# Optimization experiments

Hardware: AMD Instinct MI355X
Metric: run time of the kernel (lower is better)

The kernel has to match this reference:

```python
import jax, jax.numpy as jnp
import numpy as np

N = 2048
RESTITUTION = 0.5
EPS = 1e-12


def setup_inputs() -> dict:
    key = jax.random.key(0)
    k1, k2, k3, k4 = jax.random.split(key, 4)
    pos = jax.random.uniform(k1, (N, 2), jnp.float32, 0.0, 200.0)
    rad = jax.random.uniform(k2, (N,), jnp.float32, 0.5, 2.0)
    vel = jax.random.normal(k3, (N, 2), jnp.float32)
    mass = jax.random.uniform(k4, (N,), jnp.float32, 0.5, 2.0)
    return {"pos": pos, "rad": rad, "vel": vel, "mass": mass, "seed": 0}


def _forward(pos, rad, vel, mass, seed):
    rkey = jax.random.key(seed)
    skey = jax.random.split(rkey)[0]  # mirrors skey = jr.split(rkey)[0]
    # ---- pairwise circle-vs-circle contact tests, lower triangle i > j ----
    d = pos[:, None, :] - pos[None, :, :]            # [N,N,2], vector j -> i
    dist = jnp.sqrt(jnp.sum(d * d, -1) + EPS)        # [N,N]
    pen = (rad[:, None] + rad[None, :]) - dist       # penetration depth
    tri = jnp.arange(N)[:, None] > jnp.arange(N)[None, :]
    valid = (pen > 0.0) & tri                        # i < j pairs are nan'd in original
    normal = d / dist[..., None]
    pen_vec_raw = normal * pen[..., None]            # [N,N,2]
    cp_raw = 0.5 * (pos[:, None, :] + pos[None, :, :])  # contact point (midpoint)
    # scatter counts of non-nan contacts (computed in original, unused downstream)
    counts = valid.astype(jnp.int32)
    # ---- bernoulli(0.5)-gated recording into all_contacts ----
    skey = jax.random.split(skey)[0]
    gkey, _ = jax.random.split(skey)
    gate = jax.random.bernoulli(gkey, 0.5, (N, N))
    keep = valid & gate
    all_pen = jnp.where(keep[..., None], pen_vec_raw, 0.0)   # init zeros
    all_cp = jnp.where(keep[..., None], cp_raw, jnp.nan)     # init nan
    # ---- per-row uniform random choice among recorded (non-nan) contacts ----
    ok = ~jnp.any(jnp.isnan(all_cp), axis=-1)        # [N,N]
    n_ok = jnp.sum(ok, axis=-1)                      # [N]
    logits = jnp.where(ok, 0.0, -jnp.inf)
    keys = jax.random.split(skey, N)
    sampled = jax.vmap(jax.random.categorical)(keys, logits)  # uniform over valid
    rows = jnp.arange(N)
    chosen_j = jnp.where(n_ok == 0, rows, sampled)   # fall back to self (skipped)
    pen_sel = all_pen[rows, chosen_j]                # [N,2]
    cp_sel = all_cp[rows, chosen_j]                  # [N,2]
    inv_m = 1.0 / mass

    # ---- sequential collision resolution (scatter updates into SoA) ----
    def step(carry, x):
        p, v = carry
        i, j, pv, cp = x
        upd = (i != j) & ~jnp.any(jnp.isnan(cp))
        pi, pj = p[i], p[j]
        vi, vj = v[i], v[j]
        imi, imj = inv_m[i], inv_m[j]
        nrm = pv / (jnp.sqrt(jnp.sum(pv * pv) + EPS))
        corr = pv / (imi + imj)                      # positional de-penetration
        new_pi = pi + corr * imi
        new_pj = pj - corr * imj
        vrel = jnp.dot(vi - vj, nrm)
        jimp = jnp.where(vrel < 0.0, -(1.0 + RESTITUTION) * vrel / (imi + imj), 0.0)
        new_vi = vi + jimp * imi * nrm
        new_vj = vj - jimp * imj * nrm
        p = p.at[i].set(jnp.where(upd, new_pi, pi))
        p = p.at[j].set(jnp.where(upd, new_pj, pj))
        v = v.at[i].set(jnp.where(upd, new_vi, vi))
        v = v.at[j].set(jnp.where(upd, new_vj, vj))
        return (p, v), None

    (pos_out, vel_out), _ = jax.lax.scan(step, (pos, vel), (rows, chosen_j, pen_sel, cp_sel))
    return jnp.concatenate([pos_out, vel_out], axis=-1)  # [N,4]


def reference(pos, rad, vel, mass, seed):
    return _forward(pos, rad, vel, mass, seed)
```

## Files before the change

kernel.cpp:

```cpp
#include <hip/hip_runtime.h>
#include <stdint.h>

#define NPART 2048
#define FEPS 1e-12f
#define PARTITIONABLE 1

__device__ __forceinline__ uint32_t rotl32(uint32_t v, uint32_t r) {
  return (v << r) | (v >> (32u - r));
}

__device__ __forceinline__ void tf2x32(uint32_t k0, uint32_t k1,
                                       uint32_t x0, uint32_t x1,
                                       uint32_t& o0, uint32_t& o1) {
  uint32_t ks2 = k0 ^ k1 ^ 0x1BD11BDAu;
#define TF_RND(r) { x0 += x1; x1 = rotl32(x1, r); x1 ^= x0; }
  x0 += k0; x1 += k1;
  TF_RND(13u) TF_RND(15u) TF_RND(26u) TF_RND(6u)
  x0 += k1; x1 += ks2 + 1u;
  TF_RND(17u) TF_RND(29u) TF_RND(16u) TF_RND(24u)
  x0 += ks2; x1 += k0 + 2u;
  TF_RND(13u) TF_RND(15u) TF_RND(26u) TF_RND(6u)
  x0 += k0; x1 += k1 + 3u;
  TF_RND(17u) TF_RND(29u) TF_RND(16u) TF_RND(24u)
  x0 += k1; x1 += ks2 + 4u;
  TF_RND(13u) TF_RND(15u) TF_RND(26u) TF_RND(6u)
  x0 += ks2; x1 += k0 + 5u;
#undef TF_RND
  o0 = x0; o1 = x1;
}

__device__ __forceinline__ void split_first(uint32_t k0, uint32_t k1,
                                            uint32_t& o0, uint32_t& o1) {
#if PARTITIONABLE
  tf2x32(k0, k1, 0u, 0u, o0, o1);
#else
  uint32_t a0, a1, b0, b1;
  tf2x32(k0, k1, 0u, 2u, a0, a1);
  tf2x32(k0, k1, 1u, 3u, b0, b1);
  o0 = a0; o1 = b0;
#endif
}

__device__ __forceinline__ void split_at(uint32_t k0, uint32_t k1, uint32_t M,
                                         uint32_t r, uint32_t& o0, uint32_t& o1) {
#if PARTITIONABLE
  tf2x32(k0, k1, 0u, r, o0, o1);
#else
  uint32_t c0 = 2u * r, c1 = 2u * r + 1u;
  uint32_t a0, a1;
  if (c0 < M) { tf2x32(k0, k1, c0, c0 + M, a0, a1); o0 = a0; }
  else        { tf2x32(k0, k1, c0 - M, c0, a0, a1); o0 = a1; }
  if (c1 < M) { tf2x32(k0, k1, c1, c1 + M, a0, a1); o1 = a0; }
  else        { tf2x32(k0, k1, c1 - M, c1, a0, a1); o1 = a1; }
#endif
}

__device__ __forceinline__ uint32_t bits_at(uint32_t k0, uint32_t k1,
                                            uint32_t S_half, uint32_t idx) {
  uint32_t a0, a1;
#if PARTITIONABLE
  (void)S_half;
  tf2x32(k0, k1, 0u, idx, a0, a1);
  return a0 ^ a1;
#else
  if (idx < S_half) { tf2x32(k0, k1, idx, idx + S_half, a0, a1); return a0; }
  else              { tf2x32(k0, k1, idx - S_half, idx, a0, a1); return a1; }
#endif
}

__device__ __forceinline__ void derive_keys(int seed, uint32_t& g0, uint32_t& g1,
                                            uint32_t& s0, uint32_t& s1) {
  uint64_t sv = (uint64_t)(int64_t)seed;
  uint32_t k0 = (uint32_t)(sv >> 32), k1 = (uint32_t)sv;
  uint32_t a0, a1;
  split_first(k0, k1, a0, a1);
  split_first(a0, a1, s0, s1);
  split_first(s0, s1, g0, g1);
}

__global__ __launch_bounds__(256) void phase1_choose(
    const float* __restrict__ pos, const float* __restrict__ rad,
    const int* __restrict__ seedp, int* __restrict__ chosen,
    float* __restrict__ pen_out) {
#pragma clang fp contract(off)
  const int lane = threadIdx.x & 63;
  const int i = blockIdx.x * 4 + (threadIdx.x >> 6);

  uint32_t g0, g1, s0, s1;
  derive_keys(seedp[0], g0, g1, s0, s1);
  uint32_t ki0, ki1;
  split_at(s0, s1, (uint32_t)NPART, (uint32_t)i, ki0, ki1);

  const float pix = pos[2 * i], piy = pos[2 * i + 1];
  const float ri = rad[i];

  unsigned long long best = 0ull;
  for (int j = lane; j < i; j += 64) {
    float2 pj = reinterpret_cast<const float2*>(pos)[j];
    float dx = pix - pj.x;
    float dy = piy - pj.y;
    float dist = sqrtf(dx * dx + dy * dy + FEPS);
    float pen = (ri + rad[j]) - dist;
    if (pen > 0.0f) {
      uint32_t gb = bits_at(g0, g1, (uint32_t)NPART * NPART / 2u,
                            (uint32_t)(i * NPART + j));
      if ((gb >> 31) == 0u) {
        uint32_t b = bits_at(ki0, ki1, (uint32_t)NPART / 2u, (uint32_t)j);
        unsigned long long cand =
            ((unsigned long long)(b >> 9) << 32) |
            (uint32_t)(0xFFFFFFFFu - (uint32_t)j);
        if (cand > best) best = cand;
      }
    }
  }
  for (int off = 1; off < 64; off <<= 1) {
    unsigned long long o = __shfl_xor(best, off, 64);
    if (o > best) best = o;
  }
  if (lane == 0) {
    if (best == 0ull) {
      chosen[i] = -1;
      pen_out[2 * i] = 0.0f;
      pen_out[2 * i + 1] = 0.0f;
    } else {
      int j = (int)(0xFFFFFFFFu - (uint32_t)(best & 0xFFFFFFFFu));
      float2 pj = reinterpret_cast<const float2*>(pos)[j];
      float dx = pix - pj.x;
      float dy = piy - pj.y;
      float dist = sqrtf(dx * dx + dy * dy + FEPS);
      float pen = (ri + rad[j]) - dist;
      chosen[i] = j;
      pen_out[2 * i] = (dx / dist) * pen;
      pen_out[2 * i + 1] = (dy / dist) * pen;
    }
  }
}

__global__ __launch_bounds__(256) void phase2_scan(
    const float* __restrict__ pos, const float* __restrict__ vel,
    const float* __restrict__ mass, const int* __restrict__ chosen,
    const float* __restrict__ pen, float* __restrict__ out) {
#pragma clang fp contract(off)
  __shared__ float px[NPART], py[NPART], vx[NPART], vy[NPART];
  __shared__ int list_[NPART], cjl[NPART];
  __shared__ float Ax[NPART], Ay[NPART], Bx[NPART], By[NPART];
  __shared__ float nx_[NPART], ny_[NPART], ss[NPART], imi_[NPART], imj_[NPART];
  __shared__ int minK[NPART];
  __shared__ unsigned char done[NPART];
  __shared__ int cnts[256];
  __shared__ int total, remaining;

  const int tid = threadIdx.x;
  for (int r = tid; r < NPART; r += 256) {
    float2 p2 = reinterpret_cast<const float2*>(pos)[r];
    float2 v2 = reinterpret_cast<const float2*>(vel)[r];
    px[r] = p2.x; py[r] = p2.y;
    vx[r] = v2.x; vy[r] = v2.y;
  }

  const int base = tid * 8;
  int loc[8];
  int c = 0;
#pragma unroll
  for (int t = 0; t < 8; ++t) {
    loc[t] = chosen[base + t];
    if (loc[t] >= 0) c++;
  }
  cnts[tid] = c;
  __syncthreads();
  for (int off = 1; off < 256; off <<= 1) {
    int v = 0;
    if (tid >= off) v = cnts[tid - off];
    __syncthreads();
    cnts[tid] += v;
    __syncthreads();
  }
  int excl = cnts[tid] - c;
  if (tid == 255) total = cnts[255];
  __syncthreads();
  {
    int w = excl;
#pragma unroll
    for (int t = 0; t < 8; ++t) {
      if (loc[t] >= 0) { list_[w] = base + t; cjl[w] = loc[t]; w++; }
    }
  }
  __syncthreads();
  const int K = total;

  for (int k = tid; k < K; k += 256) {
    int i = list_[k], j = cjl[k];
    float imi = 1.0f / mass[i];
    float imj = 1.0f / mass[j];
    float s = imi + imj;
    float pvx = pen[2 * i], pvy = pen[2 * i + 1];
    float nn = sqrtf(pvx * pvx + pvy * pvy + FEPS);
    Ax[k] = (pvx / s) * imi; Ay[k] = (pvy / s) * imi;
    Bx[k] = (pvx / s) * imj; By[k] = (pvy / s) * imj;
    nx_[k] = pvx / nn; ny_[k] = pvy / nn;
    ss[k] = s; imi_[k] = imi; imj_[k] = imj;
  }
  for (int k = tid; k < K; k += 256) done[k] = 0;
  if (tid == 0) remaining = K;
  __syncthreads();

  for (int round = 0; round < NPART; ++round) {
    for (int p = tid; p < NPART; p += 256) minK[p] = 0x7FFFFFFF;
    __syncthreads();
    for (int k = tid; k < K; k += 256) {
      if (!done[k]) {
        atomicMin(&minK[list_[k]], k);
        atomicMin(&minK[cjl[k]], k);
      }
    }
    __syncthreads();
    for (int k = tid; k < K; k += 256) {
      if (!done[k]) {
        int i = list_[k], j = cjl[k];
        if (minK[i] == k && minK[j] == k) {
          px[i] = px[i] + Ax[k]; py[i] = py[i] + Ay[k];
          px[j] = px[j] - Bx[k]; py[j] = py[j] - By[k];
          float rx = vx[i] - vx[j], ry = vy[i] - vy[j];
          float vrel = rx * nx_[k] + ry * ny_[k];
          if (vrel < 0.0f) {
            float jimp = (-1.5f * vrel) / ss[k];
            float ji = jimp * imi_[k], jj = jimp * imj_[k];
            vx[i] = vx[i] + ji * nx_[k]; vy[i] = vy[i] + ji * ny_[k];
            vx[j] = vx[j] - jj * nx_[k]; vy[j] = vy[j] - jj * ny_[k];
          }
          done[k] = 1;
          atomicSub(&remaining, 1);
        }
      }
    }
    __syncthreads();
    if (remaining == 0) break;
  }

  for (int r = tid; r < NPART; r += 256) {
    float4 o;
    o.x = px[r]; o.y = py[r]; o.z = vx[r]; o.w = vy[r];
    reinterpret_cast<float4*>(out)[r] = o;
  }
}

extern "C" void kernel_launch(void* const* d_in, const int* in_sizes, int n_in,
                              void* d_out, int out_size, void* d_ws, size_t ws_size,
                              hipStream_t stream) {
  const float* pos = (const float*)d_in[0];
  const float* rad = (const float*)d_in[1];
  const float* vel = (const float*)d_in[2];
  const float* mass = (const float*)d_in[3];
  const int* seed = (const int*)d_in[4];

  int* chosen = (int*)d_ws;
  float* pen = (float*)((char*)d_ws + NPART * sizeof(int));

  phase1_choose<<<dim3(NPART / 4), dim3(256), 0, stream>>>(pos, rad, seed,
                                                           chosen, pen);
  phase2_scan<<<dim3(1), dim3(256), 0, stream>>>(pos, vel, mass, chosen, pen,
                                                 (float*)d_out);
}
```

Before: 85.27 us.

## Run collision rounds in a single wavefront with round-tagged atomics

Phase 2 now runs the conflict-free round scheduling in one 64-lane wavefront, so the per-round block barriers and minK reset are replaced by round-tagged atomicMax and a wave vote. Shared arrays are packed into float2/float4 and a combined i|j index, and the block prefix scan is replaced with wave shuffles. Phase 1 remaps rows so each block handles rows spread across the triangle, to balance work per block. The active-set bitmask only covers up to 32 slots per lane, which caps K at 2048, and only one wave does the update work.

New measurement: 83.94 us. About the same (-1.6%).

```diff
diff --git a/kernel.cpp b/kernel.cpp
--- a/kernel.cpp
+++ b/kernel.cpp
@@ -84,7 +84,7 @@
     float* __restrict__ pen_out) {
 #pragma clang fp contract(off)
   const int lane = threadIdx.x & 63;
-  const int i = blockIdx.x * 4 + (threadIdx.x >> 6);
+  const int i = blockIdx.x + 512 * (threadIdx.x >> 6);
 
   uint32_t g0, g1, s0, s1;
   derive_keys(seedp[0], g0, g1, s0, s1);
@@ -141,106 +141,121 @@
     const float* __restrict__ mass, const int* __restrict__ chosen,
     const float* __restrict__ pen, float* __restrict__ out) {
 #pragma clang fp contract(off)
-  __shared__ float px[NPART], py[NPART], vx[NPART], vy[NPART];
-  __shared__ int list_[NPART], cjl[NPART];
-  __shared__ float Ax[NPART], Ay[NPART], Bx[NPART], By[NPART];
-  __shared__ float nx_[NPART], ny_[NPART], ss[NPART], imi_[NPART], imj_[NPART];
+  __shared__ float2 pxy[NPART], vxy[NPART];
+  __shared__ int ij[NPART];
+  __shared__ float4 PA[NPART];
+  __shared__ float4 PB[NPART];
   __shared__ int minK[NPART];
-  __shared__ unsigned char done[NPART];
-  __shared__ int cnts[256];
-  __shared__ int total, remaining;
+  __shared__ int wsum[4];
 
   const int tid = threadIdx.x;
+  const int lane = tid & 63, w = tid >> 6;
+
   for (int r = tid; r < NPART; r += 256) {
-    float2 p2 = reinterpret_cast<const float2*>(pos)[r];
-    float2 v2 = reinterpret_cast<const float2*>(vel)[r];
-    px[r] = p2.x; py[r] = p2.y;
-    vx[r] = v2.x; vy[r] = v2.y;
+    pxy[r] = reinterpret_cast<const float2*>(pos)[r];
+    vxy[r] = reinterpret_cast<const float2*>(vel)[r];
+    minK[r] = 0;
   }
 
   const int base = tid * 8;
-  int loc[8];
+  int4 c0 = reinterpret_cast<const int4*>(chosen)[2 * tid];
+  int4 c1 = reinterpret_cast<const int4*>(chosen)[2 * tid + 1];
+  int loc[8] = {c0.x, c0.y, c0.z, c0.w, c1.x, c1.y, c1.z, c1.w};
   int c = 0;
 #pragma unroll
-  for (int t = 0; t < 8; ++t) {
-    loc[t] = chosen[base + t];
-    if (loc[t] >= 0) c++;
-  }
-  cnts[tid] = c;
-  __syncthreads();
-  for (int off = 1; off < 256; off <<= 1) {
-    int v = 0;
-    if (tid >= off) v = cnts[tid - off];
-    __syncthreads();
-    cnts[tid] += v;
-    __syncthreads();
-  }
-  int excl = cnts[tid] - c;
-  if (tid == 255) total = cnts[255];
-  __syncthreads();
+  for (int t = 0; t < 8; ++t) c += (loc[t] >= 0);
+
+  int incl = c;
+#pragma unroll
+  for (int off = 1; off < 64; off <<= 1) {
+    int v = __shfl_up(incl, off, 64);
+    if (lane >= off) incl += v;
+  }
+  if (lane == 63) wsum[w] = incl;
+  __syncthreads();
+  int woff = 0, K = 0;
+#pragma unroll
+  for (int q = 0; q < 4; ++q) {
+    int s = wsum[q];
+    if (q < w) woff += s;
+    K += s;
+  }
   {
-    int w = excl;
+    int wr = woff + incl - c;
 #pragma unroll
     for (int t = 0; t < 8; ++t) {
-      if (loc[t] >= 0) { list_[w] = base + t; cjl[w] = loc[t]; w++; }
-    }
-  }
-  __syncthreads();
-  const int K = total;
+      if (loc[t] >= 0) { ij[wr] = ((base + t) << 16) | loc[t]; wr++; }
+    }
+  }
+  __syncthreads();
 
   for (int k = tid; k < K; k += 256) {
-    int i = list_[k], j = cjl[k];
+    int pr = ij[k];
+    int i = pr >> 16, j = pr & 0xFFFF;
     float imi = 1.0f / mass[i];
     float imj = 1.0f / mass[j];
     float s = imi + imj;
     float pvx = pen[2 * i], pvy = pen[2 * i + 1];
     float nn = sqrtf(pvx * pvx + pvy * pvy + FEPS);
-    Ax[k] = (pvx / s) * imi; Ay[k] = (pvy / s) * imi;
-    Bx[k] = (pvx / s) * imj; By[k] = (pvy / s) * imj;
-    nx_[k] = pvx / nn; ny_[k] = pvy / nn;
-    ss[k] = s; imi_[k] = imi; imj_[k] = imj;
-  }
-  for (int k = tid; k < K; k += 256) done[k] = 0;
-  if (tid == 0) remaining = K;
-  __syncthreads();
-
-  for (int round = 0; round < NPART; ++round) {
-    for (int p = tid; p < NPART; p += 256) minK[p] = 0x7FFFFFFF;
-    __syncthreads();
-    for (int k = tid; k < K; k += 256) {
-      if (!done[k]) {
-        atomicMin(&minK[list_[k]], k);
-        atomicMin(&minK[cjl[k]], k);
-      }
-    }
-    __syncthreads();
-    for (int k = tid; k < K; k += 256) {
-      if (!done[k]) {
-        int i = list_[k], j = cjl[k];
-        if (minK[i] == k && minK[j] == k) {
-          px[i] = px[i] + Ax[k]; py[i] = py[i] + Ay[k];
-          px[j] = px[j] - Bx[k]; py[j] = py[j] - By[k];
-          float rx = vx[i] - vx[j], ry = vy[i] - vy[j];
-          float vrel = rx * nx_[k] + ry * ny_[k];
-          if (vrel < 0.0f) {
-            float jimp = (-1.5f * vrel) / ss[k];
-            float ji = jimp * imi_[k], jj = jimp * imj_[k];
-            vx[i] = vx[i] + ji * nx_[k]; vy[i] = vy[i] + ji * ny_[k];
-            vx[j] = vx[j] - jj * nx_[k]; vy[j] = vy[j] - jj * ny_[k];
-          }
-          done[k] = 1;
-          atomicSub(&remaining, 1);
+    PA[k] = make_float4((pvx / s) * imi, (pvy / s) * imi,
+                        (pvx / s) * imj, (pvy / s) * imj);
+    PB[k] = make_float4(pvx / nn, pvy / nn, imi, imj);
+  }
+  __syncthreads();
+
+  if (w == 0) {
+    const int RMAX = (K + 63) >> 6;
+    uint32_t act = 0;
+    for (int r = 0; r < RMAX; ++r)
+      if (r * 64 + lane < K) act |= (1u << r);
+
+    for (int round = 1; act || __any(act); ++round) {
+      int tagbase = round << 12;
+      for (int r = 0; r < RMAX; ++r) {
+        if (act & (1u << r)) {
+          int k = r * 64 + lane;
+          int pr = ij[k];
+          int tag = tagbase | (4095 - k);
+          atomicMax(&minK[pr >> 16], tag);
+          atomicMax(&minK[pr & 0xFFFF], tag);
         }
       }
-    }
-    __syncthreads();
-    if (remaining == 0) break;
-  }
+      __threadfence_block();
+      for (int r = 0; r < RMAX; ++r) {
+        if (act & (1u << r)) {
+          int k = r * 64 + lane;
+          int pr = ij[k];
+          int i = pr >> 16, j = pr & 0xFFFF;
+          int tag = tagbase | (4095 - k);
+          if (minK[i] == tag && minK[j] == tag) {
+            float4 pa = PA[k], pb = PB[k];
+            float2 pi = pxy[i], pj = pxy[j];
+            pxy[i] = make_float2(pi.x + pa.x, pi.y + pa.y);
+            pxy[j] = make_float2(pj.x - pa.z, pj.y - pa.w);
+            float2 vi = vxy[i], vj = vxy[j];
+            float rx = vi.x - vj.x, ry = vi.y - vj.y;
+            float vrel = rx * pb.x + ry * pb.y;
+            if (vrel < 0.0f) {
+              float s = pb.z + pb.w;
+              float jimp = (-1.5f * vrel) / s;
+              float ji = jimp * pb.z, jj = jimp * pb.w;
+              vxy[i] = make_float2(vi.x + ji * pb.x, vi.y + ji * pb.y);
+              vxy[j] = make_float2(vj.x - jj * pb.x, vj.y - jj * pb.y);
+            }
+            act &= ~(1u << r);
+          }
+        }
+      }
+      __threadfence_block();
+      if (!__any(act)) break;
+      if (round > NPART) break;
+    }
+  }
+  __syncthreads();
 
   for (int r = tid; r < NPART; r += 256) {
-    float4 o;
-    o.x = px[r]; o.y = py[r]; o.z = vx[r]; o.w = vy[r];
-    reinterpret_cast<float4*>(out)[r] = o;
+    float2 p2 = pxy[r], v2 = vxy[r];
+    reinterpret_cast<float4*>(out)[r] = make_float4(p2.x, p2.y, v2.x, v2.y);
   }
 }
 
@@ -256,8 +271,7 @@
   int* chosen = (int*)d_ws;
   float* pen = (float*)((char*)d_ws + NPART * sizeof(int));
 
-  phase1_choose<<<dim3(NPART / 4), dim3(256), 0, stream>>>(pos, rad, seed,
-                                                           chosen, pen);
+  phase1_choose<<<dim3(512), dim3(256), 0, stream>>>(pos, rad, seed, chosen, pen);
   phase2_scan<<<dim3(1), dim3(256), 0, stream>>>(pos, vel, mass, chosen, pen,
                                                  (float*)d_out);
 }
```
